# Kernel tuning notes

Hardware: AMD Instinct MI355X
Metric: run time of the kernel (lower is better)

The kernel has to match this reference:

```python
import jax, jax.numpy as jnp
import numpy as np
from jax import lax

DIM = 128
HEADS = 4
HEAD_DIM = DIM // HEADS          # 32
SR = 2
BN_EPS = 1e-5


def setup_inputs() -> dict:
    key = jax.random.key(0)
    ks = jax.random.split(key, 16)
    B, N, C = 8, 3136, DIM
    H = W = 56
    Nkv = (H // SR) * (W // SR)  # 784
    s = 0.05
    inp = {
        "x": jax.random.normal(ks[0], (B, N, C), jnp.float32),
        "relative_pos": jax.random.normal(ks[1], (HEADS, N, Nkv), jnp.float32),
        "Wq": jax.random.normal(ks[2], (C, C), jnp.float32) * s,
        "bq": jnp.zeros((C,), jnp.float32),
        "Wk": jax.random.normal(ks[3], (C, C), jnp.float32) * s,
        "bk": jnp.zeros((C,), jnp.float32),
        "Wv": jax.random.normal(ks[4], (C, C), jnp.float32) * s,
        "bv": jnp.zeros((C,), jnp.float32),
        "conv_w": jax.random.normal(ks[5], (C, 1, SR, SR), jnp.float32) * s,  # depthwise OIHW
        "conv_b": jnp.zeros((C,), jnp.float32),
        "bn_gamma": jnp.ones((C,), jnp.float32),
        "bn_beta": jnp.zeros((C,), jnp.float32),
        "bn_mean": jax.random.normal(ks[6], (C,), jnp.float32) * 0.1,
        "bn_var": jax.random.uniform(ks[7], (C,), jnp.float32, 0.5, 1.5),
        "Wp": jax.random.normal(ks[8], (C, C), jnp.float32) * s,
        "bp": jnp.zeros((C,), jnp.float32),
        "H": H,
        "W": W,
    }
    return inp


def reference(x, relative_pos, Wq, bq, Wk, bk, Wv, bv, conv_w, conv_b,
              bn_gamma, bn_beta, bn_mean, bn_var, Wp, bp, H, W):
    B, N, C = x.shape
    scale = HEAD_DIM ** -0.5

    # q: (B, heads, N, head_dim)
    q = (x @ Wq + bq).reshape(B, N, HEADS, HEAD_DIM).transpose(0, 2, 1, 3)

    # spatial reduction: depthwise conv stride SR + BatchNorm (eval, running stats)
    x_img = x.transpose(0, 2, 1).reshape(B, C, H, W)
    y = lax.conv_general_dilated(
        x_img, conv_w, window_strides=(SR, SR), padding="VALID",
        feature_group_count=C,
        dimension_numbers=("NCHW", "OIHW", "NCHW")) + conv_b[None, :, None, None]
    inv = bn_gamma * lax.rsqrt(bn_var + BN_EPS)
    y = y * inv[None, :, None, None] + (bn_beta - bn_mean * inv)[None, :, None, None]
    x_ = y.reshape(B, C, -1).transpose(0, 2, 1)  # (B, Nkv, C)
    Nkv = x_.shape[1]

    k = (x_ @ Wk + bk).reshape(B, Nkv, HEADS, HEAD_DIM).transpose(0, 2, 1, 3)
    v = (x_ @ Wv + bv).reshape(B, Nkv, HEADS, HEAD_DIM).transpose(0, 2, 1, 3)

    attn = jnp.einsum("bhnd,bhmd->bhnm", q, k) * scale + relative_pos[None]
    attn = jax.nn.softmax(attn, axis=-1)
    out = jnp.einsum("bhnm,bhmd->bhnd", attn, v)
    out = out.transpose(0, 2, 1, 3).reshape(B, N, C)
    return out @ Wp + bp
```

## Files before the change

### kernel.cpp

```cpp
#include <hip/hip_runtime.h>
#include <hip/hip_bf16.h>

#define BATCH 8
#define NQ 3136
#define CDIM 128
#define NHEAD 4
#define HD 32
#define NKV 784
#define HIMG 56
#define SCALE 0.17677669529663687f

typedef __attribute__((ext_vector_type(8))) short bf8_t;
typedef __attribute__((ext_vector_type(4))) float f4_t;

using bf16 = __hip_bfloat16;
using u16  = unsigned short;

static __device__ __forceinline__ float b2f(bf16 v){ return __bfloat162float(v); }
static __device__ __forceinline__ bf16  f2b(float v){ return __float2bfloat16(v); }
static __device__ __forceinline__ short f2s(float v){
  union { bf16 b; short s; } u; u.b = f2b(v); return u.s;
}
static __device__ __forceinline__ float ld1(const void* p, size_t i, int f){
  return f ? b2f(((const bf16*)p)[i]) : ((const float*)p)[i];
}
static __device__ __forceinline__ bf8_t ld8(const void* p, size_t i, int f){
  if (f) return *(const bf8_t*)((const bf16*)p + i);
  const float* fp = (const float*)p + i;
  float4 a = *(const float4*)fp;
  float4 b = *(const float4*)(fp + 4);
  bf8_t r;
  r[0]=f2s(a.x); r[1]=f2s(a.y); r[2]=f2s(a.z); r[3]=f2s(a.w);
  r[4]=f2s(b.x); r[5]=f2s(b.y); r[6]=f2s(b.z); r[7]=f2s(b.w);
  return r;
}
static __device__ __forceinline__ int detect_flag(const void* var_raw){
  const u16* h = (const u16*)var_raw;
  int lane = threadIdx.x & 63;
  bool ok = true;
  #pragma unroll
  for (int t = 0; t < 2; t++){
    union { u16 u; bf16 b; } cv; cv.u = h[lane + 64*t];
    float v = b2f(cv.b);
    ok = ok && (v > 0.3f) && (v < 1.7f);
  }
  return (__ballot(ok) == ~0ull) ? 1 : 0;
}

static __device__ __forceinline__ void mfma_row(
    const bf8_t a[4], const bf16* __restrict__ Wt, int m, int g, f4_t acc[8])
{
  #pragma unroll
  for (int ct = 0; ct < 8; ct++){
    f4_t c = {0.f,0.f,0.f,0.f};
    const bf16* bp = Wt + (size_t)(ct*16 + m)*CDIM + 8*g;
    #pragma unroll
    for (int ks = 0; ks < 4; ks++){
      bf8_t b = *(const bf8_t*)(bp + 32*ks);
      c = __builtin_amdgcn_mfma_f32_16x16x32_bf16(a[ks], b, c, 0,0,0);
    }
    acc[ct] = c;
  }
}

__global__ __launch_bounds__(256) void prep_kernel(
    const void* __restrict__ Wq, const void* __restrict__ Wk,
    const void* __restrict__ Wv, const void* __restrict__ Wp,
    const void* __restrict__ var, const void* __restrict__ cw,
    const void* __restrict__ cb, const void* __restrict__ gam,
    const void* __restrict__ bet, const void* __restrict__ mea,
    const void* __restrict__ bq, const void* __restrict__ bk,
    const void* __restrict__ bv, const void* __restrict__ bp,
    bf16* __restrict__ Wqt, bf16* __restrict__ Wkt,
    bf16* __restrict__ Wvt, bf16* __restrict__ Wpt,
    bf16* __restrict__ bqs, bf16* __restrict__ bks,
    bf16* __restrict__ bvs, bf16* __restrict__ bps,
    float* __restrict__ cwf, float* __restrict__ inv, float* __restrict__ shift2)
{
  int f = detect_flag(var);
  int idx = blockIdx.x*256 + threadIdx.x;
  int mat = idx >> 14;
  int e   = idx & 16383;
  int o = e >> 7, i = e & 127;
  const void* src; bf16* dst; float s = 1.f;
  if      (mat == 0){ src = Wq; dst = Wqt; s = SCALE; }
  else if (mat == 1){ src = Wk; dst = Wkt; }
  else if (mat == 2){ src = Wv; dst = Wvt; }
  else              { src = Wp; dst = Wpt; }
  dst[e] = f2b(ld1(src, (size_t)i*128 + o, f) * s);

  if (blockIdx.x == 0){
    int t = threadIdx.x;
    cwf[t]       = ld1(cw, t, f);
    cwf[t + 256] = ld1(cw, t + 256, f);
    if (t < 128){
      bqs[t] = f2b(ld1(bq, t, f) * SCALE);
      bks[t] = f2b(ld1(bk, t, f));
      bvs[t] = f2b(ld1(bv, t, f));
      bps[t] = f2b(ld1(bp, t, f));
      float iv = ld1(gam, t, f) * rsqrtf(ld1(var, t, f) + 1e-5f);
      inv[t] = iv;
      shift2[t] = ld1(bet, t, f) - ld1(mea, t, f) * iv + ld1(cb, t, f) * iv;
    }
  }
}

__global__ __launch_bounds__(256) void fat_kernel(
    const void* __restrict__ x, const void* __restrict__ var,
    const float* __restrict__ cwf, const float* __restrict__ inv,
    const float* __restrict__ shift2, bf16* __restrict__ xr,
    const bf16* __restrict__ Wqt, const bf16* __restrict__ bqs,
    bf16* __restrict__ qbf)
{
  int f = detect_flag(var);
  if (blockIdx.x < 3136){
    int idx = blockIdx.x*256 + threadIdx.x;
    int c  = idx & 127;
    int t  = idx >> 7;
    int b  = t / NKV;
    int kv = t - b*NKV;
    int i = kv/28, j = kv - i*28;
    size_t base = (size_t)(b*NQ + 2*i*HIMG + 2*j)*CDIM + c;
    float acc = ld1(x, base, f)                   * cwf[c*4 + 0]
              + ld1(x, base + CDIM, f)            * cwf[c*4 + 1]
              + ld1(x, base + HIMG*CDIM, f)       * cwf[c*4 + 2]
              + ld1(x, base + HIMG*CDIM + CDIM, f)* cwf[c*4 + 3];
    xr[idx] = f2b(acc * inv[c] + shift2[c]);
  } else {
    int wave = threadIdx.x >> 6, lane = threadIdx.x & 63;
    int m = lane & 15, g = lane >> 4;
    int task = (blockIdx.x - 3136)*4 + wave;
    int row0 = task*16;
    bf8_t a[4];
    #pragma unroll
    for (int ks = 0; ks < 4; ks++)
      a[ks] = ld8(x, (size_t)(row0 + m)*CDIM + 8*g + 32*ks, f);
    f4_t acc[8];
    mfma_row(a, Wqt, m, g, acc);
    #pragma unroll
    for (int ct = 0; ct < 8; ct++){
      int col = ct*16 + m;
      float bv = b2f(bqs[col]);
      #pragma unroll
      for (int r = 0; r < 4; r++)
        qbf[(size_t)(row0 + 4*g + r)*CDIM + col] = f2b(acc[ct][r] + bv);
    }
  }
}

__global__ __launch_bounds__(256) void kv_kernel(
    const bf16* __restrict__ xr,
    const bf16* __restrict__ Wkt, const bf16* __restrict__ Wvt,
    const bf16* __restrict__ bks, const bf16* __restrict__ bvs,
    bf16* __restrict__ kbf, bf16* __restrict__ vtb)
{
  int wave = threadIdx.x >> 6, lane = threadIdx.x & 63;
  int m = lane & 15, g = lane >> 4;
  bool isK = blockIdx.x < 98;
  int bx = isK ? blockIdx.x : blockIdx.x - 98;
  int row0 = (bx*4 + wave)*16;
  bf8_t a[4];
  #pragma unroll
  for (int ks = 0; ks < 4; ks++)
    a[ks] = *(const bf8_t*)(xr + (size_t)(row0 + m)*CDIM + 8*g + 32*ks);
  f4_t acc[8];
  mfma_row(a, isK ? Wkt : Wvt, m, g, acc);

  if (isK){
    #pragma unroll
    for (int ct = 0; ct < 8; ct++){
      int col = ct*16 + m;
      float bv = b2f(bks[col]);
      #pragma unroll
      for (int r = 0; r < 4; r++)
        kbf[(size_t)(row0 + 4*g + r)*CDIM + col] = f2b(acc[ct][r] + bv);
    }
  } else {
    int b   = row0 / NKV;
    int kv0 = row0 - b*NKV + 4*g;
    #pragma unroll
    for (int ct = 0; ct < 8; ct++){
      int col = ct*16 + m;
      float bv = b2f(bvs[col]);
      int h = col >> 5, d = col & 31;
      union { bf16 hh[4]; uint2 u; } pk;
      #pragma unroll
      for (int r = 0; r < 4; r++) pk.hh[r] = f2b(acc[ct][r] + bv);
      *(uint2*)(vtb + (size_t)((b*NHEAD + h)*HD + d)*NKV + kv0) = pk.u;
    }
  }
}

template<int W>
static __device__ __forceinline__ void stage_rel(
    const void* __restrict__ rel, int f, bf16* __restrict__ rel_l,
    size_t rowbase, int kv0)
{
  const int tid = threadIdx.x;
  if (f){
    constexpr int PER = W/8;
    constexpr int SL  = 64*PER;
    #pragma unroll
    for (int it = 0; it < (SL + 255)/256; it++){
      int s0 = it*256 + tid;
      if (SL < 256 && s0 >= SL) continue;
      int row = s0 / PER;
      int col = (s0 - row*PER)*8;
      const bf16* gp = (const bf16*)rel + (rowbase + row)*NKV + kv0 + col;
      uint2 lo = *(const uint2*)gp;
      uint2 hi = *(const uint2*)(gp + 4);
      *(uint2*)(rel_l + row*132 + col)     = lo;
      *(uint2*)(rel_l + row*132 + col + 4) = hi;
    }
  } else {
    constexpr int PER = W/4;
    constexpr int SL  = 64*PER;
    #pragma unroll
    for (int it = 0; it < (SL + 255)/256; it++){
      int s0 = it*256 + tid;
      int row = s0 / PER;
      int col = (s0 - row*PER)*4;
      const float* gp = (const float*)rel + (rowbase + row)*NKV + kv0 + col;
      float4 v = *(const float4*)gp;
      union { u16 hh[4]; uint2 u; } pk;
      pk.hh[0]=(u16)f2s(v.x); pk.hh[1]=(u16)f2s(v.y);
      pk.hh[2]=(u16)f2s(v.z); pk.hh[3]=(u16)f2s(v.w);
      *(uint2*)(rel_l + row*132 + col) = pk.u;
    }
  }
}

template<int T>
static __device__ __forceinline__ void attn_chunk(
    int kv0, const bf16* __restrict__ kbase,
    const bf16* __restrict__ vb0, const bf16* __restrict__ vb1,
    const bf16* __restrict__ rel_l, int wrow, bf16* pl, int m, int g,
    bf8_t q8, float m_run[4], float l_run[4], f4_t& O0, f4_t& O1)
{
  f4_t s[T];
  #pragma unroll
  for (int t = 0; t < T; t++){
    bf8_t k8 = *(const bf8_t*)(kbase + (size_t)(kv0 + t*16)*CDIM);
    f4_t z = {0.f,0.f,0.f,0.f};
    s[t] = __builtin_amdgcn_mfma_f32_16x16x32_bf16(q8, k8, z, 0,0,0);
  }
  #pragma unroll
  for (int t = 0; t < T; t++){
    #pragma unroll
    for (int r = 0; r < 4; r++)
      s[t][r] += b2f(rel_l[(wrow + 4*g + r)*132 + t*16 + m]);
  }
  float mloc[4];
  #pragma unroll
  for (int r = 0; r < 4; r++){
    float v = s[0][r];
    #pragma unroll
    for (int t = 1; t < T; t++) v = fmaxf(v, s[t][r]);
    mloc[r] = v;
  }
  #pragma unroll
  for (int xm = 1; xm < 16; xm <<= 1){
    #pragma unroll
    for (int r = 0; r < 4; r++)
      mloc[r] = fmaxf(mloc[r], __shfl_xor(mloc[r], xm, 64));
  }
  #pragma unroll
  for (int r = 0; r < 4; r++){
    float mn = fmaxf(m_run[r], mloc[r]);
    float al = __expf(m_run[r] - mn);
    m_run[r] = mn;
    l_run[r] *= al;
    O0[r] *= al; O1[r] *= al;
  }
  #pragma unroll
  for (int t = 0; t < T; t++){
    #pragma unroll
    for (int r = 0; r < 4; r++){
      float p = __expf(s[t][r] - m_run[r]);
      l_run[r] += p;
      pl[(4*g + r)*136 + t*16 + m] = f2b(p);
    }
  }
  __syncthreads();
  constexpr int NKS = (T + 1)/2;
  #pragma unroll
  for (int ks = 0; ks < NKS; ks++){
    bf8_t a8 = *(const bf8_t*)(pl + m*136 + ks*32 + 8*g);
    bf8_t v0, v1;
    if (T == 1 && g >= 2){
      bf8_t z8 = {0,0,0,0,0,0,0,0};
      a8 = z8; v0 = z8; v1 = z8;
    } else {
      v0 = *(const bf8_t*)(vb0 + kv0 + ks*32 + 8*g);
      v1 = *(const bf8_t*)(vb1 + kv0 + ks*32 + 8*g);
    }
    O0 = __builtin_amdgcn_mfma_f32_16x16x32_bf16(a8, v0, O0, 0,0,0);
    O1 = __builtin_amdgcn_mfma_f32_16x16x32_bf16(a8, v1, O1, 0,0,0);
  }
}

template<int QF>
__global__ __launch_bounds__(256) void attn_kernel(
    const bf16* __restrict__ qbf, const void* __restrict__ x,
    const bf16* __restrict__ Wqt, const bf16* __restrict__ bqs,
    const bf16* __restrict__ kb, const bf16* __restrict__ vtb,
    const void* __restrict__ rel, const void* __restrict__ var,
    void* __restrict__ dout, bf16* __restrict__ obf)
{
  int f = detect_flag(var);
  int wave = threadIdx.x >> 6, lane = threadIdx.x & 63;
  int m = lane & 15, g = lane >> 4;
  int b = blockIdx.z, h = blockIdx.y, qt = blockIdx.x;
  int qrow0 = qt*64 + wave*16;
  int wrow  = wave*16;

  __shared__ bf16 rel_l[64*132];
  __shared__ bf16 Plds[4][16*136];
  bf16* pl = Plds[wave];

  bf8_t q8;
  if constexpr (QF == 0){
    q8 = *(const bf8_t*)(qbf + (size_t)(b*NQ + qrow0 + m)*CDIM + h*HD + 8*g);
  } else {
    bf8_t xa[4];
    #pragma unroll
    for (int ks = 0; ks < 4; ks++)
      xa[ks] = ld8(x, (size_t)(b*NQ + qrow0 + m)*CDIM + 8*g + 32*ks, f);
    f4_t qc0 = {0.f,0.f,0.f,0.f}, qc1 = {0.f,0.f,0.f,0.f};
    const bf16* wp0 = Wqt + (size_t)(h*HD + m)*CDIM + 8*g;
    const bf16* wp1 = Wqt + (size_t)(h*HD + 16 + m)*CDIM + 8*g;
    #pragma unroll
    for (int ks = 0; ks < 4; ks++){
      bf8_t w0 = *(const bf8_t*)(wp0 + 32*ks);
      bf8_t w1 = *(const bf8_t*)(wp1 + 32*ks);
      qc0 = __builtin_amdgcn_mfma_f32_16x16x32_bf16(xa[ks], w0, qc0, 0,0,0);
      qc1 = __builtin_amdgcn_mfma_f32_16x16x32_bf16(xa[ks], w1, qc1, 0,0,0);
    }
    float bv0 = b2f(bqs[h*HD + m]);
    float bv1 = b2f(bqs[h*HD + 16 + m]);
    #pragma unroll
    for (int r = 0; r < 4; r++){
      pl[(4*g + r)*136 + m]      = f2b(qc0[r] + bv0);
      pl[(4*g + r)*136 + 16 + m] = f2b(qc1[r] + bv1);
    }
    q8 = *(const bf8_t*)(pl + m*136 + 8*g);
  }

  const bf16* kbase = kb  + (size_t)(b*NKV + m)*CDIM + h*HD + 8*g;
  const bf16* vb0   = vtb + (size_t)((b*NHEAD + h)*HD + m)*NKV;
  const bf16* vb1   = vtb + (size_t)((b*NHEAD + h)*HD + 16 + m)*NKV;
  size_t rowbase = (size_t)h*NQ + qt*64;

  float m_run[4], l_run[4];
  f4_t O0 = {0.f,0.f,0.f,0.f}, O1 = {0.f,0.f,0.f,0.f};
  #pragma unroll
  for (int r = 0; r < 4; r++){ m_run[r] = -1e30f; l_run[r] = 0.f; }

  #pragma unroll 1
  for (int kv0 = 0; kv0 < 768; kv0 += 128){
    stage_rel<128>(rel, f, rel_l, rowbase, kv0);
    __syncthreads();
    attn_chunk<8>(kv0, kbase, vb0, vb1, rel_l, wrow, pl, m, g, q8, m_run, l_run, O0, O1);
  }
  stage_rel<16>(rel, f, rel_l, rowbase, 768);
  __syncthreads();
  attn_chunk<1>(768, kbase, vb0, vb1, rel_l, wrow, pl, m, g, q8, m_run, l_run, O0, O1);

  #pragma unroll
  for (int xm = 1; xm < 16; xm <<= 1){
    #pragma unroll
    for (int r = 0; r < 4; r++)
      l_run[r] += __shfl_xor(l_run[r], xm, 64);
  }
  bf16* ob = f ? (bf16*)dout : obf;
  size_t orow = (size_t)(b*NQ + qrow0 + 4*g);
  #pragma unroll
  for (int r = 0; r < 4; r++){
    float iv = 1.0f / l_run[r];
    ob[(orow + r)*CDIM + h*HD + m]      = f2b(O0[r] * iv);
    ob[(orow + r)*CDIM + h*HD + 16 + m] = f2b(O1[r] * iv);
  }
}

__global__ __launch_bounds__(256) void proj_kernel(
    const bf16* A0, const bf16* A1, const bf16* __restrict__ Wt,
    const bf16* __restrict__ bias, void* outp, const void* __restrict__ var)
{
  int f = detect_flag(var);
  const bf16* A = f ? A0 : A1;
  int wave = threadIdx.x >> 6, lane = threadIdx.x & 63;
  int m = lane & 15, g = lane >> 4;
  int row0 = (blockIdx.x*4 + wave)*16;
  bf8_t a[4];
  #pragma unroll
  for (int ks = 0; ks < 4; ks++)
    a[ks] = *(const bf8_t*)(A + (size_t)(row0 + m)*CDIM + 8*g + 32*ks);
  f4_t acc[8];
  mfma_row(a, Wt, m, g, acc);
  #pragma unroll
  for (int ct = 0; ct < 8; ct++){
    int col = ct*16 + m;
    float bv = b2f(bias[col]);
    #pragma unroll
    for (int r = 0; r < 4; r++){
      size_t oi = (size_t)(row0 + 4*g + r)*CDIM + col;
      float v = acc[ct][r] + bv;
      if (f) ((bf16*)outp)[oi]  = f2b(v);
      else   ((float*)outp)[oi] = v;
    }
  }
}

extern "C" void kernel_launch(void* const* d_in, const int* in_sizes, int n_in,
                              void* d_out, int out_size, void* d_ws, size_t ws_size,
                              hipStream_t stream)
{
  const void* x   = d_in[0];
  const void* rel = d_in[1];
  const void* Wq  = d_in[2];
  const void* bq  = d_in[3];
  const void* Wk  = d_in[4];
  const void* bk  = d_in[5];
  const void* Wv  = d_in[6];
  const void* bv  = d_in[7];
  const void* cw  = d_in[8];
  const void* cb  = d_in[9];
  const void* gam = d_in[10];
  const void* bet = d_in[11];
  const void* mea = d_in[12];
  const void* var = d_in[13];
  const void* Wp  = d_in[14];
  const void* bp  = d_in[15];

  char* w = (char*)d_ws;
  auto alloc = [&](size_t bytes){
    char* p = w; w += (bytes + 255) & ~(size_t)255; return p;
  };
  bf16* Wqt = (bf16*)alloc(128*128*sizeof(bf16));
  bf16* Wkt = (bf16*)alloc(128*128*sizeof(bf16));
  bf16* Wvt = (bf16*)alloc(128*128*sizeof(bf16));
  bf16* Wpt = (bf16*)alloc(128*128*sizeof(bf16));
  bf16* bqs = (bf16*)alloc(128*sizeof(bf16));
  bf16* bks = (bf16*)alloc(128*sizeof(bf16));
  bf16* bvs = (bf16*)alloc(128*sizeof(bf16));
  bf16* bps = (bf16*)alloc(128*sizeof(bf16));
  float* cwf    = (float*)alloc(512*sizeof(float));
  float* inv    = (float*)alloc(128*sizeof(float));
  float* shift2 = (float*)alloc(128*sizeof(float));
  bf16* xr  = (bf16*)alloc((size_t)BATCH*NKV*CDIM*sizeof(bf16));
  bf16* kbf = (bf16*)alloc((size_t)BATCH*NKV*CDIM*sizeof(bf16));
  bf16* vtb = (bf16*)alloc((size_t)BATCH*NKV*CDIM*sizeof(bf16));
  bf16* obf = (bf16*)alloc((size_t)BATCH*NQ*CDIM*sizeof(bf16));

  size_t qbf_bytes = (size_t)BATCH*NQ*CDIM*sizeof(bf16);
  bool use_q = (size_t)(((char*)d_ws + ws_size) - w) >= qbf_bytes + 256;
  bf16* qbf = use_q ? (bf16*)alloc(qbf_bytes) : nullptr;

  prep_kernel<<<256, 256, 0, stream>>>(Wq, Wk, Wv, Wp, var, cw, cb, gam, bet, mea,
                                       bq, bk, bv, bp,
                                       Wqt, Wkt, Wvt, Wpt, bqs, bks, bvs, bps,
                                       cwf, inv, shift2);
  fat_kernel<<<3136 + (use_q ? 392 : 0), 256, 0, stream>>>(
      x, var, cwf, inv, shift2, xr, Wqt, bqs, qbf);
  kv_kernel<<<196, 256, 0, stream>>>(xr, Wkt, Wvt, bks, bvs, kbf, vtb);
  if (use_q)
    attn_kernel<0><<<dim3(49, NHEAD, BATCH), 256, 0, stream>>>(
        qbf, x, Wqt, bqs, kbf, vtb, rel, var, d_out, obf);
  else
    attn_kernel<1><<<dim3(49, NHEAD, BATCH), 256, 0, stream>>>(
        qbf, x, Wqt, bqs, kbf, vtb, rel, var, d_out, obf);
  proj_kernel<<<392, 256, 0, stream>>>((const bf16*)d_out, obf, Wpt, bps, d_out, var);
}
```

Before: 245.2 us.

## Pre-convert relative_pos to bf16 and read it directly with batch-major attention grid

Adds extra blocks to fat_kernel that convert the fp32 relative_pos bias into a bf16 workspace copy once per call. The attention kernel no longer stages the bias through shared memory; each lane reads its bias values straight from global memory, which also drops the block-wide barriers. The grid is reordered so that batch is the fastest-varying index: the eight batches sharing the same (head, query tile) bias slice run back to back and can reuse it from L2. The trade-offs are an extra write and read of the converted bias, and per-lane global loads that are less coalesced than the old staged copy.

```diff
diff --git a/kernel.cpp b/kernel.cpp
--- a/kernel.cpp
+++ b/kernel.cpp
@@ -110,7 +110,8 @@
     const float* __restrict__ cwf, const float* __restrict__ inv,
     const float* __restrict__ shift2, bf16* __restrict__ xr,
     const bf16* __restrict__ Wqt, const bf16* __restrict__ bqs,
-    bf16* __restrict__ qbf)
+    bf16* __restrict__ qbf,
+    const void* __restrict__ rel, bf16* __restrict__ relb, int qblk)
 {
   int f = detect_flag(var);
   if (blockIdx.x < 3136){
@@ -126,7 +127,7 @@
               + ld1(x, base + HIMG*CDIM, f)       * cwf[c*4 + 2]
               + ld1(x, base + HIMG*CDIM + CDIM, f)* cwf[c*4 + 3];
     xr[idx] = f2b(acc * inv[c] + shift2[c]);
-  } else {
+  } else if ((int)blockIdx.x < 3136 + qblk){
     int wave = threadIdx.x >> 6, lane = threadIdx.x & 63;
     int m = lane & 15, g = lane >> 4;
     int task = (blockIdx.x - 3136)*4 + wave;
@@ -145,6 +146,19 @@
       for (int r = 0; r < 4; r++)
         qbf[(size_t)(row0 + 4*g + r)*CDIM + col] = f2b(acc[ct][r] + bv);
     }
+  } else {
+    if (f) return;
+    int bi = blockIdx.x - 3136 - qblk;
+    size_t gid = ((size_t)bi*256 + threadIdx.x)*8;
+    const float* fp = (const float*)rel + gid;
+    float4 a  = *(const float4*)fp;
+    float4 b4 = *(const float4*)(fp + 4);
+    union { u16 hh[8]; uint4 u4; } pk;
+    pk.hh[0]=(u16)f2s(a.x);  pk.hh[1]=(u16)f2s(a.y);
+    pk.hh[2]=(u16)f2s(a.z);  pk.hh[3]=(u16)f2s(a.w);
+    pk.hh[4]=(u16)f2s(b4.x); pk.hh[5]=(u16)f2s(b4.y);
+    pk.hh[6]=(u16)f2s(b4.z); pk.hh[7]=(u16)f2s(b4.w);
+    *(uint4*)(relb + gid) = pk.u4;
   }
 }
 
@@ -191,50 +205,11 @@
   }
 }
 
-template<int W>
-static __device__ __forceinline__ void stage_rel(
-    const void* __restrict__ rel, int f, bf16* __restrict__ rel_l,
-    size_t rowbase, int kv0)
-{
-  const int tid = threadIdx.x;
-  if (f){
-    constexpr int PER = W/8;
-    constexpr int SL  = 64*PER;
-    #pragma unroll
-    for (int it = 0; it < (SL + 255)/256; it++){
-      int s0 = it*256 + tid;
-      if (SL < 256 && s0 >= SL) continue;
-      int row = s0 / PER;
-      int col = (s0 - row*PER)*8;
-      const bf16* gp = (const bf16*)rel + (rowbase + row)*NKV + kv0 + col;
-      uint2 lo = *(const uint2*)gp;
-      uint2 hi = *(const uint2*)(gp + 4);
-      *(uint2*)(rel_l + row*132 + col)     = lo;
-      *(uint2*)(rel_l + row*132 + col + 4) = hi;
-    }
-  } else {
-    constexpr int PER = W/4;
-    constexpr int SL  = 64*PER;
-    #pragma unroll
-    for (int it = 0; it < (SL + 255)/256; it++){
-      int s0 = it*256 + tid;
-      int row = s0 / PER;
-      int col = (s0 - row*PER)*4;
-      const float* gp = (const float*)rel + (rowbase + row)*NKV + kv0 + col;
-      float4 v = *(const float4*)gp;
-      union { u16 hh[4]; uint2 u; } pk;
-      pk.hh[0]=(u16)f2s(v.x); pk.hh[1]=(u16)f2s(v.y);
-      pk.hh[2]=(u16)f2s(v.z); pk.hh[3]=(u16)f2s(v.w);
-      *(uint2*)(rel_l + row*132 + col) = pk.u;
-    }
-  }
-}
-
-template<int T>
+template<int T, int RM>
 static __device__ __forceinline__ void attn_chunk(
     int kv0, const bf16* __restrict__ kbase,
     const bf16* __restrict__ vb0, const bf16* __restrict__ vb1,
-    const bf16* __restrict__ rel_l, int wrow, bf16* pl, int m, int g,
+    const void* __restrict__ relp, bf16* pl, int m, int g,
     bf8_t q8, float m_run[4], float l_run[4], f4_t& O0, f4_t& O1)
 {
   f4_t s[T];
@@ -247,8 +222,11 @@
   #pragma unroll
   for (int t = 0; t < T; t++){
     #pragma unroll
-    for (int r = 0; r < 4; r++)
-      s[t][r] += b2f(rel_l[(wrow + 4*g + r)*132 + t*16 + m]);
+    for (int r = 0; r < 4; r++){
+      int ri = r*NKV + kv0 + t*16;
+      float rv = RM ? b2f(((const bf16*)relp)[ri]) : ((const float*)relp)[ri];
+      s[t][r] += rv;
+    }
   }
   float mloc[4];
   #pragma unroll
@@ -281,7 +259,6 @@
       pl[(4*g + r)*136 + t*16 + m] = f2b(p);
     }
   }
-  __syncthreads();
   constexpr int NKS = (T + 1)/2;
   #pragma unroll
   for (int ks = 0; ks < NKS; ks++){
@@ -304,17 +281,16 @@
     const bf16* __restrict__ qbf, const void* __restrict__ x,
     const bf16* __restrict__ Wqt, const bf16* __restrict__ bqs,
     const bf16* __restrict__ kb, const bf16* __restrict__ vtb,
-    const void* __restrict__ rel, const void* __restrict__ var,
+    const void* __restrict__ rel, const bf16* __restrict__ relb,
+    const void* __restrict__ var,
     void* __restrict__ dout, bf16* __restrict__ obf)
 {
   int f = detect_flag(var);
   int wave = threadIdx.x >> 6, lane = threadIdx.x & 63;
   int m = lane & 15, g = lane >> 4;
-  int b = blockIdx.z, h = blockIdx.y, qt = blockIdx.x;
+  int b = blockIdx.x, qt = blockIdx.y, h = blockIdx.z;
   int qrow0 = qt*64 + wave*16;
-  int wrow  = wave*16;
-
-  __shared__ bf16 rel_l[64*132];
+
   __shared__ bf16 Plds[4][16*136];
   bf16* pl = Plds[wave];
 
@@ -349,22 +325,26 @@
   const bf16* kbase = kb  + (size_t)(b*NKV + m)*CDIM + h*HD + 8*g;
   const bf16* vb0   = vtb + (size_t)((b*NHEAD + h)*HD + m)*NKV;
   const bf16* vb1   = vtb + (size_t)((b*NHEAD + h)*HD + 16 + m)*NKV;
-  size_t rowbase = (size_t)h*NQ + qt*64;
+  size_t roff = ((size_t)h*NQ + qt*64 + wave*16 + 4*g)*NKV + m;
 
   float m_run[4], l_run[4];
   f4_t O0 = {0.f,0.f,0.f,0.f}, O1 = {0.f,0.f,0.f,0.f};
   #pragma unroll
   for (int r = 0; r < 4; r++){ m_run[r] = -1e30f; l_run[r] = 0.f; }
 
-  #pragma unroll 1
-  for (int kv0 = 0; kv0 < 768; kv0 += 128){
-    stage_rel<128>(rel, f, rel_l, rowbase, kv0);
-    __syncthreads();
-    attn_chunk<8>(kv0, kbase, vb0, vb1, rel_l, wrow, pl, m, g, q8, m_run, l_run, O0, O1);
-  }
-  stage_rel<16>(rel, f, rel_l, rowbase, 768);
-  __syncthreads();
-  attn_chunk<1>(768, kbase, vb0, vb1, rel_l, wrow, pl, m, g, q8, m_run, l_run, O0, O1);
+  if (f || relb != nullptr){
+    const bf16* rp = (f ? (const bf16*)rel : relb) + roff;
+    #pragma unroll 1
+    for (int kv0 = 0; kv0 < 768; kv0 += 128)
+      attn_chunk<8,1>(kv0, kbase, vb0, vb1, rp, pl, m, g, q8, m_run, l_run, O0, O1);
+    attn_chunk<1,1>(768, kbase, vb0, vb1, rp, pl, m, g, q8, m_run, l_run, O0, O1);
+  } else {
+    const float* rp = (const float*)rel + roff;
+    #pragma unroll 1
+    for (int kv0 = 0; kv0 < 768; kv0 += 128)
+      attn_chunk<8,0>(kv0, kbase, vb0, vb1, rp, pl, m, g, q8, m_run, l_run, O0, O1);
+    attn_chunk<1,0>(768, kbase, vb0, vb1, rp, pl, m, g, q8, m_run, l_run, O0, O1);
+  }
 
   #pragma unroll
   for (int xm = 1; xm < 16; xm <<= 1){
@@ -452,22 +432,31 @@
   bf16* vtb = (bf16*)alloc((size_t)BATCH*NKV*CDIM*sizeof(bf16));
   bf16* obf = (bf16*)alloc((size_t)BATCH*NQ*CDIM*sizeof(bf16));
 
+  size_t relb_bytes = (size_t)NHEAD*NQ*NKV*sizeof(bf16);
+  bf16* relb = nullptr;
+  if (((char*)d_ws + ws_size) - w >= (ptrdiff_t)(relb_bytes + 256))
+    relb = (bf16*)alloc(relb_bytes);
+
   size_t qbf_bytes = (size_t)BATCH*NQ*CDIM*sizeof(bf16);
-  bool use_q = (size_t)(((char*)d_ws + ws_size) - w) >= qbf_bytes + 256;
+  bool use_q = (((char*)d_ws + ws_size) - w) >= (ptrdiff_t)(qbf_bytes + 256);
   bf16* qbf = use_q ? (bf16*)alloc(qbf_bytes) : nullptr;
+
+  int qblk = use_q ? 392 : 0;
+  int rblk = relb  ? 4802 : 0;
 
   prep_kernel<<<256, 256, 0, stream>>>(Wq, Wk, Wv, Wp, var, cw, cb, gam, bet, mea,
                                        bq, bk, bv, bp,
                                        Wqt, Wkt, Wvt, Wpt, bqs, bks, bvs, bps,
                                        cwf, inv, shift2);
-  fat_kernel<<<3136 + (use_q ? 392 : 0), 256, 0, stream>>>(
-      x, var, cwf, inv, shift2, xr, Wqt, bqs, qbf);
+  fat_kernel<<<3136 + qblk + rblk, 256, 0, stream>>>(
+      x, var, cwf, inv, shift2, xr, Wqt, bqs, qbf, rel, relb, qblk);
   kv_kernel<<<196, 256, 0, stream>>>(xr, Wkt, Wvt, bks, bvs, kbf, vtb);
+  dim3 ag(BATCH, 49, NHEAD);
   if (use_q)
-    attn_kernel<0><<<dim3(49, NHEAD, BATCH), 256, 0, stream>>>(
-        qbf, x, Wqt, bqs, kbf, vtb, rel, var, d_out, obf);
+    attn_kernel<0><<<ag, 256, 0, stream>>>(
+        qbf, x, Wqt, bqs, kbf, vtb, rel, relb, var, d_out, obf);
   else
-    attn_kernel<1><<<dim3(49, NHEAD, BATCH), 256, 0, stream>>>(
-        qbf, x, Wqt, bqs, kbf, vtb, rel, var, d_out, obf);
+    attn_kernel<1><<<ag, 256, 0, stream>>>(
+        qbf, x, Wqt, bqs, kbf, vtb, rel, relb, var, d_out, obf);
   proj_kernel<<<392, 256, 0, stream>>>((const bf16*)d_out, obf, Wpt, bps, d_out, var);
 }
```

Measured after the change: 307.2 us. +25.3%, slower.
